# Performance work log

Measured on AMD Instinct MI355X. Metric: run time of the kernel, lower is better.

## Reference

```python
import jax, jax.numpy as jnp
import numpy as np

D_IN, D_K, D_V, BLOCK = 1024, 64, 64, 2048
B, T = 4, 2048

def setup_inputs() -> dict:
    key = jax.random.key(0)
    k0, k1, k2, k3 = jax.random.split(key, 4)
    x = jax.random.normal(k0, (B, T, D_IN), dtype=jnp.float32)
    s = 1.0 / np.sqrt(D_IN)
    Wq = jax.random.normal(k1, (D_IN, D_K), dtype=jnp.float32) * s
    Wk = jax.random.normal(k2, (D_IN, D_K), dtype=jnp.float32) * s
    Wv = jax.random.normal(k3, (D_IN, D_V), dtype=jnp.float32) * s
    return {"x": x, "Wq": Wq, "Wk": Wk, "Wv": Wv}

def reference(x, Wq, Wk, Wv):
    # Q,K,V projections (Linear without bias)
    Q = jnp.einsum('btc,ck->btk', x, Wq)
    K = jnp.einsum('btc,ck->btk', x, Wk)
    V = jnp.einsum('btc,cv->btv', x, Wv)
    Tq = x.shape[1]
    scores = jnp.einsum('bqk,btk->bqt', Q, K)  # [B,T,T]
    causal = jnp.tril(jnp.ones((Tq, Tq), dtype=bool))
    scores = jnp.where(causal, scores, -jnp.inf)
    attn = jax.nn.softmax(scores, axis=-1)
    # NOTE: original divides the AV product by sqrt(d_k) AFTER softmax
    out = jnp.einsum('bqt,btv->bqv', attn, V) / jnp.sqrt(jnp.asarray(K.shape[-1], dtype=x.dtype))
    return out
```

## Files before the change

### kernel.cpp

```cpp
#include <hip/hip_runtime.h>
#include <math.h>

typedef unsigned short u16;
typedef __attribute__((ext_vector_type(4))) float f32x4;
typedef __bf16 bf16x8 __attribute__((ext_vector_type(8)));

#define MFMA16(a,b,c) __builtin_amdgcn_mfma_f32_16x16x32_bf16((a),(b),(c),0,0,0)

typedef const __attribute__((address_space(1))) unsigned GU;
typedef __attribute__((address_space(3))) unsigned LU;
__device__ __forceinline__ void gl_lds16(const void* g, void* l) {
    __builtin_amdgcn_global_load_lds((GU*)g, (LU*)l, 16, 0, 0);
}

__device__ __forceinline__ u16 f2b(float f) {
    __bf16 h = (__bf16)f;
    return __builtin_bit_cast(u16, h);
}
__device__ __forceinline__ float b2f(u16 u) {
    unsigned v = (unsigned)u << 16;
    return __builtin_bit_cast(float, v);
}

__global__ __launch_bounds__(128) void wtrans_kernel(
    const float* __restrict__ Wq, const float* __restrict__ Wk,
    const float* __restrict__ Wv, u16* __restrict__ Wt2)
{
    const int n = blockIdx.x;
    const float* W = (n < 64) ? Wq : ((n < 128) ? Wk : Wv);
    const int nc = n & 63, cg = n >> 4, r = n & 15;
    const int t = threadIdx.x;
    const int k0 = t * 8;
    const int kstep = k0 >> 6, kh = (k0 >> 5) & 1, kg = (k0 >> 3) & 3;
    u16 hh[8], ll[8];
#pragma unroll
    for (int i = 0; i < 8; ++i) {
        const float a = W[(size_t)(k0 + i) * 64 + nc];
        hh[i] = f2b(a);
        ll[i] = f2b(a - b2f(hh[i]));
    }
    const size_t fi = (((size_t)kstep * 12 + cg) * 2 + kh) * 2;
    u16* dst = Wt2 + fi * 512 + kg * 128 + r * 8;
    uint4 vh, vl;
    vh.x = (uint)hh[0] | ((uint)hh[1] << 16); vh.y = (uint)hh[2] | ((uint)hh[3] << 16);
    vh.z = (uint)hh[4] | ((uint)hh[5] << 16); vh.w = (uint)hh[6] | ((uint)hh[7] << 16);
    vl.x = (uint)ll[0] | ((uint)ll[1] << 16); vl.y = (uint)ll[2] | ((uint)ll[3] << 16);
    vl.z = (uint)ll[4] | ((uint)ll[5] << 16); vl.w = (uint)ll[6] | ((uint)ll[7] << 16);
    *(uint4*)dst         = vh;
    *(uint4*)(dst + 512) = vl;
}

__global__ __launch_bounds__(512, 2) void proj_kernel(
    const float* __restrict__ x, const u16* __restrict__ Wt2,
    u16* __restrict__ Qhi, u16* __restrict__ Qlo,
    u16* __restrict__ Khi, u16* __restrict__ Klo, u16* __restrict__ Vt)
{
    __shared__ u16 WB[2][24576];
    __shared__ u16 vs[32][72];

    const int t = threadIdx.x, w = t >> 6, lane = t & 63;
    const int lo = lane & 15, hi = lane >> 4;
    const int mh = w & 1, nt = w >> 1;
    const int row0 = blockIdx.x * 32;

    f32x4 acc[3];
#pragma unroll
    for (int i = 0; i < 3; ++i) acc[i] = (f32x4){0.f, 0.f, 0.f, 0.f};

    const float* xrow = x + (size_t)(row0 + mh * 16 + lo) * 1024 + hi * 8;

    auto stage = [&](int buf, int step) {
        const u16* src = Wt2 + (size_t)step * 24576 + (size_t)(w * 6) * 512 + (size_t)lane * 8;
        u16* dst = &WB[buf][(w * 6) * 512];
#pragma unroll
        for (int i = 0; i < 6; ++i)
            gl_lds16(src + i * 512, dst + i * 512);
    };
    auto loadXf = [&](float4 (&xv)[2][2], int step) {
#pragma unroll
        for (int kh = 0; kh < 2; ++kh) {
            xv[kh][0] = *(const float4*)(xrow + step * 64 + kh * 32);
            xv[kh][1] = *(const float4*)(xrow + step * 64 + kh * 32 + 4);
        }
    };
    auto compute = [&](int buf, const float4 (&xv)[2][2]) {
        bf16x8 ah[2], al[2];
#pragma unroll
        for (int kh = 0; kh < 2; ++kh)
#pragma unroll
            for (int j = 0; j < 2; ++j)
#pragma unroll
                for (int c = 0; c < 4; ++c) {
                    const float f = (&xv[kh][j].x)[c];
                    const __bf16 h = (__bf16)f;
                    ah[kh][j * 4 + c] = h;
                    al[kh][j * 4 + c] = (__bf16)(f - (float)h);
                }
        const char* base = (const char*)&WB[buf][0];
#pragma unroll
        for (int i = 0; i < 3; ++i) {
            const int cg = nt * 3 + i;
#pragma unroll
            for (int kh = 0; kh < 2; ++kh) {
                const int fb = ((cg * 2 + kh) * 2) * 1024;
                const bf16x8 wh = *(const bf16x8*)(base + fb + lane * 16);
                const bf16x8 wl = *(const bf16x8*)(base + fb + 1024 + lane * 16);
                acc[i] = MFMA16(ah[kh], wh, acc[i]);
                acc[i] = MFMA16(ah[kh], wl, acc[i]);
                acc[i] = MFMA16(al[kh], wh, acc[i]);
            }
        }
    };

    float4 xA[2][2], xB[2][2];
    stage(0, 0);
    loadXf(xA, 0);
    __syncthreads();
    int buf = 0;
    for (int step = 0; step < 16; ++step) {
        if (step < 15) { stage(buf ^ 1, step + 1); loadXf(xB, step + 1); }
        compute(buf, xA);
        __syncthreads();
        if (step < 15) {
#pragma unroll
            for (int kh = 0; kh < 2; ++kh) { xA[kh][0] = xB[kh][0]; xA[kh][1] = xB[kh][1]; }
        }
        buf ^= 1;
    }

#pragma unroll
    for (int i = 0; i < 3; ++i) {
        const int cg = nt * 3 + i;
#pragma unroll
        for (int r = 0; r < 4; ++r) {
            const float v = acc[i][r];
            const int row = row0 + mh * 16 + hi * 4 + r;
            const u16 h = f2b(v);
            if (cg < 4) {
                Qhi[(size_t)row * 64 + cg * 16 + lo] = h;
                Qlo[(size_t)row * 64 + cg * 16 + lo] = f2b(v - b2f(h));
            } else if (cg < 8) {
                Khi[(size_t)row * 64 + (cg - 4) * 16 + lo] = h;
                Klo[(size_t)row * 64 + (cg - 4) * 16 + lo] = f2b(v - b2f(h));
            } else {
                vs[mh * 16 + hi * 4 + r][(cg - 8) * 16 + lo] = h;
            }
        }
    }
    __syncthreads();
    {
        const int bb = row0 >> 11, tok0 = row0 & 2047;
        const int d = t >> 3, part = t & 7;
        u16 tmp[4];
#pragma unroll
        for (int i = 0; i < 4; ++i) tmp[i] = vs[part * 4 + i][d];
        uint2 v2;
        v2.x = (uint)tmp[0] | ((uint)tmp[1] << 16);
        v2.y = (uint)tmp[2] | ((uint)tmp[3] << 16);
        *(uint2*)(Vt + (size_t)bb * 131072 + (size_t)d * 2048 + tok0 + part * 4) = v2;
    }
}

__global__ __launch_bounds__(512, 2) void attn_kernel(
    const u16* __restrict__ Qhi, const u16* __restrict__ Qlo,
    const u16* __restrict__ Khi, const u16* __restrict__ Klo,
    const u16* __restrict__ Vt, float* __restrict__ out)
{
    __shared__ u16 P[8][16 * 64];
    __shared__ float OA[8][16][64];
    __shared__ float LS[8][16];

    const int pi = blockIdx.x, b = blockIdx.y;
    const int t = threadIdx.x, w = t >> 6, l = t & 63;
    const int lo = l & 15, hi = l >> 4;

    const u16* Qh = Qhi + (size_t)b * 131072;
    const u16* Ql = Qlo + (size_t)b * 131072;
    const u16* Kh = Khi + (size_t)b * 131072;
    const u16* Kl = Klo + (size_t)b * 131072;
    const u16* V  = Vt  + (size_t)b * 131072;

    u16* Pw = P[w];

#pragma unroll 1
    for (int phase = 0; phase < 2; ++phase) {
        const int p = phase ? pi : (127 - pi);
        const int q0 = p * 16;
        const int nt = (p >> 2) + 1;

        bf16x8 aqh[2], aql[2];
#pragma unroll
        for (int s = 0; s < 2; ++s) {
            aqh[s] = *(const bf16x8*)(Qh + (size_t)(q0 + lo) * 64 + s * 32 + hi * 8);
            aql[s] = *(const bf16x8*)(Ql + (size_t)(q0 + lo) * 64 + s * 32 + hi * 8);
        }

        f32x4 acc[4];
        float ls[4];
#pragma unroll
        for (int r = 0; r < 4; ++r) { acc[r] = (f32x4){0.f,0.f,0.f,0.f}; ls[r] = 0.f; }

        bf16x8 kh[4][2], kl[4][2];
        auto loadK = [&](int j0) {
#pragma unroll
            for (int kg = 0; kg < 4; ++kg)
#pragma unroll
                for (int s = 0; s < 2; ++s) {
                    const size_t off = (size_t)(j0 + kg * 16 + lo) * 64 + s * 32 + hi * 8;
                    kh[kg][s] = *(const bf16x8*)(Kh + off);
                    kl[kg][s] = *(const bf16x8*)(Kl + off);
                }
        };

        if (w < nt) loadK(w * 64);
#pragma unroll 1
        for (int j = w; j < nt; j += 8) {
            const int j0 = j * 64;
            bf16x8 bv[4][2];
#pragma unroll
            for (int dg = 0; dg < 4; ++dg)
#pragma unroll
                for (int s = 0; s < 2; ++s)
                    bv[dg][s] = *(const bf16x8*)(V + (size_t)(dg * 16 + lo) * 2048 + j0 + s * 32 + hi * 8);

            f32x4 S[4];
            const f32x4 zf = (f32x4){0.f,0.f,0.f,0.f};
#pragma unroll
            for (int kg = 0; kg < 4; ++kg) {
                f32x4 sv = zf;
                sv = MFMA16(aqh[0], kh[kg][0], sv);
                sv = MFMA16(aqh[1], kh[kg][1], sv);
                sv = MFMA16(aqh[0], kl[kg][0], sv);
                sv = MFMA16(aqh[1], kl[kg][1], sv);
                sv = MFMA16(aql[0], kh[kg][0], sv);
                sv = MFMA16(aql[1], kh[kg][1], sv);
                S[kg] = sv;
            }

            if (j + 8 < nt) loadK((j + 8) * 64);

            const bool dm = (j == nt - 1);
#pragma unroll
            for (int r = 0; r < 4; ++r) {
                const int row = q0 + hi * 4 + r;
                float sv0 = S[0][r], sv1 = S[1][r], sv2 = S[2][r], sv3 = S[3][r];
                if (dm) {
                    sv0 = (j0 +      lo > row) ? -INFINITY : sv0;
                    sv1 = (j0 + 16 + lo > row) ? -INFINITY : sv1;
                    sv2 = (j0 + 32 + lo > row) ? -INFINITY : sv2;
                    sv3 = (j0 + 48 + lo > row) ? -INFINITY : sv3;
                }
                const u16 u0 = f2b(__expf(sv0)), u1 = f2b(__expf(sv1));
                const u16 u2 = f2b(__expf(sv2)), u3 = f2b(__expf(sv3));
                float ps = b2f(u0) + b2f(u1) + b2f(u2) + b2f(u3);
#pragma unroll
                for (int msk = 8; msk; msk >>= 1) ps += __shfl_xor(ps, msk, 64);
                ls[r] += ps;
                const int rowL = hi * 4 + r;
                const int base = rowL * 64;
                const int sw = rowL & 7;
                Pw[base + (((0 + (lo >> 3)) ^ sw) << 3) + (lo & 7)] = u0;
                Pw[base + (((2 + (lo >> 3)) ^ sw) << 3) + (lo & 7)] = u1;
                Pw[base + (((4 + (lo >> 3)) ^ sw) << 3) + (lo & 7)] = u2;
                Pw[base + (((6 + (lo >> 3)) ^ sw) << 3) + (lo & 7)] = u3;
            }
            const bf16x8 pa0 = *(const bf16x8*)&Pw[lo * 64 + (((hi    ) ^ (lo & 7)) << 3)];
            const bf16x8 pa1 = *(const bf16x8*)&Pw[lo * 64 + (((hi + 4) ^ (lo & 7)) << 3)];
#pragma unroll
            for (int dg = 0; dg < 4; ++dg) {
                acc[dg] = MFMA16(pa0, bv[dg][0], acc[dg]);
                acc[dg] = MFMA16(pa1, bv[dg][1], acc[dg]);
            }
        }

#pragma unroll
        for (int r = 0; r < 4; ++r) {
            if (lo == 0) LS[w][hi * 4 + r] = ls[r];
#pragma unroll
            for (int dg = 0; dg < 4; ++dg) OA[w][hi * 4 + r][dg * 16 + lo] = acc[dg][r];
        }
        __syncthreads();

        {
            const int row = t >> 5, c0 = (t & 31) * 2;
            float s0 = 0.f, s1 = 0.f, Lt = 0.f;
#pragma unroll
            for (int wv = 0; wv < 8; ++wv) {
                s0 += OA[wv][row][c0];
                s1 += OA[wv][row][c0 + 1];
                Lt += LS[wv][row];
            }
            const float inv = 0.125f / Lt;
            float2 o = make_float2(s0 * inv, s1 * inv);
            *(float2*)(out + ((size_t)b * 2048 + q0 + row) * 64 + c0) = o;
        }
        __syncthreads();
    }
}

extern "C" void kernel_launch(void* const* d_in, const int* in_sizes, int n_in,
                              void* d_out, int out_size, void* d_ws, size_t ws_size,
                              hipStream_t stream) {
    const float* x  = (const float*)d_in[0];
    const float* Wq = (const float*)d_in[1];
    const float* Wk = (const float*)d_in[2];
    const float* Wv = (const float*)d_in[3];
    float* outp = (float*)d_out;

    u16* Wt2 = (u16*)d_ws;
    u16* Qhi = Wt2 + 393216;
    u16* Qlo = Qhi + 524288;
    u16* Khi = Qlo + 524288;
    u16* Klo = Khi + 524288;
    u16* Vt  = Klo + 524288;

    wtrans_kernel<<<dim3(192), dim3(128), 0, stream>>>(Wq, Wk, Wv, Wt2);
    proj_kernel<<<dim3(256), dim3(512), 0, stream>>>(x, Wt2, Qhi, Qlo, Khi, Klo, Vt);
    attn_kernel<<<dim3(64, 4), dim3(512), 0, stream>>>(Qhi, Qlo, Khi, Klo, Vt, outp);
}
```

Before: 67.32 us.

## Halve projection K-step staging to cut LDS and raise occupancy

The projection kernel now stages half a K-step (32 columns) of the split hi/lo weights per iteration instead of 64. This halves the LDS double buffer to about 48KB and lets launch bounds request 4 blocks per CU instead of 2. The price is twice as many loop iterations and barriers, each with less MFMA work to hide latency behind. Register pressure may also tighten under the higher occupancy target.

```diff
diff --git a/kernel.cpp b/kernel.cpp
--- a/kernel.cpp
+++ b/kernel.cpp
@@ -2,6 +2,7 @@
 #include <math.h>
 
 typedef unsigned short u16;
+typedef unsigned int uint32;
 typedef __attribute__((ext_vector_type(4))) float f32x4;
 typedef __bf16 bf16x8 __attribute__((ext_vector_type(8)));
 
@@ -50,91 +51,82 @@
     *(uint4*)(dst + 512) = vl;
 }
 
-__global__ __launch_bounds__(512, 2) void proj_kernel(
+__global__ __launch_bounds__(512, 4) void proj_kernel(
     const float* __restrict__ x, const u16* __restrict__ Wt2,
     u16* __restrict__ Qhi, u16* __restrict__ Qlo,
     u16* __restrict__ Khi, u16* __restrict__ Klo, u16* __restrict__ Vt)
 {
-    __shared__ u16 WB[2][24576];
+    __shared__ u16 WB[2][24][512];
     __shared__ u16 vs[32][72];
 
     const int t = threadIdx.x, w = t >> 6, lane = t & 63;
     const int lo = lane & 15, hi = lane >> 4;
-    const int mh = w & 1, nt = w >> 1;
+    const int rh = w & 1, cq = w >> 1;
     const int row0 = blockIdx.x * 32;
 
     f32x4 acc[3];
 #pragma unroll
     for (int i = 0; i < 3; ++i) acc[i] = (f32x4){0.f, 0.f, 0.f, 0.f};
 
-    const float* xrow = x + (size_t)(row0 + mh * 16 + lo) * 1024 + hi * 8;
-
-    auto stage = [&](int buf, int step) {
-        const u16* src = Wt2 + (size_t)step * 24576 + (size_t)(w * 6) * 512 + (size_t)lane * 8;
-        u16* dst = &WB[buf][(w * 6) * 512];
-#pragma unroll
-        for (int i = 0; i < 6; ++i)
-            gl_lds16(src + i * 512, dst + i * 512);
+    const float* xrow = x + (size_t)(row0 + rh * 16 + lo) * 1024 + hi * 8;
+
+    auto stage = [&](int buf, int s) {
+        const int kstep = s >> 1, kh = s & 1;
+#pragma unroll
+        for (int i = 0; i < 3; ++i) {
+            const int j = w * 3 + i;
+            const int cg = j >> 1, hl = j & 1;
+            const int fi = ((kstep * 12 + cg) * 2 + kh) * 2 + hl;
+            gl_lds16(Wt2 + (size_t)fi * 512 + lane * 8, &WB[buf][j][0]);
+        }
     };
-    auto loadXf = [&](float4 (&xv)[2][2], int step) {
-#pragma unroll
-        for (int kh = 0; kh < 2; ++kh) {
-            xv[kh][0] = *(const float4*)(xrow + step * 64 + kh * 32);
-            xv[kh][1] = *(const float4*)(xrow + step * 64 + kh * 32 + 4);
-        }
+    auto loadX = [&](float4 (&xv)[2], int s) {
+        xv[0] = *(const float4*)(xrow + s * 32);
+        xv[1] = *(const float4*)(xrow + s * 32 + 4);
     };
-    auto compute = [&](int buf, const float4 (&xv)[2][2]) {
-        bf16x8 ah[2], al[2];
-#pragma unroll
-        for (int kh = 0; kh < 2; ++kh)
-#pragma unroll
-            for (int j = 0; j < 2; ++j)
-#pragma unroll
-                for (int c = 0; c < 4; ++c) {
-                    const float f = (&xv[kh][j].x)[c];
-                    const __bf16 h = (__bf16)f;
-                    ah[kh][j * 4 + c] = h;
-                    al[kh][j * 4 + c] = (__bf16)(f - (float)h);
-                }
-        const char* base = (const char*)&WB[buf][0];
+    auto compute = [&](int buf, const float4 (&xv)[2]) {
+        bf16x8 ah, al;
+#pragma unroll
+        for (int j = 0; j < 2; ++j)
+#pragma unroll
+            for (int c = 0; c < 4; ++c) {
+                const float f = (&xv[j].x)[c];
+                const __bf16 h = (__bf16)f;
+                ah[j * 4 + c] = h;
+                al[j * 4 + c] = (__bf16)(f - (float)h);
+            }
 #pragma unroll
         for (int i = 0; i < 3; ++i) {
-            const int cg = nt * 3 + i;
-#pragma unroll
-            for (int kh = 0; kh < 2; ++kh) {
-                const int fb = ((cg * 2 + kh) * 2) * 1024;
-                const bf16x8 wh = *(const bf16x8*)(base + fb + lane * 16);
-                const bf16x8 wl = *(const bf16x8*)(base + fb + 1024 + lane * 16);
-                acc[i] = MFMA16(ah[kh], wh, acc[i]);
-                acc[i] = MFMA16(ah[kh], wl, acc[i]);
-                acc[i] = MFMA16(al[kh], wh, acc[i]);
-            }
+            const int cg = cq * 3 + i;
+            const bf16x8 wh = *(const bf16x8*)((const char*)&WB[buf][cg * 2][0] + lane * 16);
+            const bf16x8 wl = *(const bf16x8*)((const char*)&WB[buf][cg * 2 + 1][0] + lane * 16);
+            acc[i] = MFMA16(ah, wh, acc[i]);
+            acc[i] = MFMA16(ah, wl, acc[i]);
+            acc[i] = MFMA16(al, wh, acc[i]);
         }
     };
 
-    float4 xA[2][2], xB[2][2];
+    float4 xA[2], xB[2];
     stage(0, 0);
-    loadXf(xA, 0);
+    loadX(xA, 0);
     __syncthreads();
     int buf = 0;
-    for (int step = 0; step < 16; ++step) {
-        if (step < 15) { stage(buf ^ 1, step + 1); loadXf(xB, step + 1); }
+#pragma unroll 1
+    for (int s = 0; s < 32; ++s) {
+        if (s < 31) { stage(buf ^ 1, s + 1); loadX(xB, s + 1); }
         compute(buf, xA);
         __syncthreads();
-        if (step < 15) {
-#pragma unroll
-            for (int kh = 0; kh < 2; ++kh) { xA[kh][0] = xB[kh][0]; xA[kh][1] = xB[kh][1]; }
-        }
+        xA[0] = xB[0]; xA[1] = xB[1];
         buf ^= 1;
     }
 
 #pragma unroll
     for (int i = 0; i < 3; ++i) {
-        const int cg = nt * 3 + i;
+        const int cg = cq * 3 + i;
 #pragma unroll
         for (int r = 0; r < 4; ++r) {
             const float v = acc[i][r];
-            const int row = row0 + mh * 16 + hi * 4 + r;
+            const int row = row0 + rh * 16 + hi * 4 + r;
             const u16 h = f2b(v);
             if (cg < 4) {
                 Qhi[(size_t)row * 64 + cg * 16 + lo] = h;
@@ -143,7 +135,7 @@
                 Khi[(size_t)row * 64 + (cg - 4) * 16 + lo] = h;
                 Klo[(size_t)row * 64 + (cg - 4) * 16 + lo] = f2b(v - b2f(h));
             } else {
-                vs[mh * 16 + hi * 4 + r][(cg - 8) * 16 + lo] = h;
+                vs[rh * 16 + hi * 4 + r][(cg - 8) * 16 + lo] = h;
             }
         }
     }
```

Measured after the change: 78.00 us. 1.16x slower.

## Triple-buffer projection K-loop with explicit vmcnt waits and batched LDS reads

Applied to the files above, without the earlier changes.

The projection kernel's weight staging moves from double to triple buffering. Global x loads and LDS weight reads are issued through inline asm, and explicit s_waitcnt vmcnt counts keep two steps of loads in flight, replacing the full __syncthreads per step with a raw s_barrier. All 12 weight fragments are read from LDS up front, before the MFMA chain runs. LDS use grows by half and the launch-bounds occupancy hint of 2 is dropped, which may lower occupancy, and the hand-counted vmcnt values are fragile.

```diff
diff --git a/kernel.cpp b/kernel.cpp
--- a/kernel.cpp
+++ b/kernel.cpp
@@ -2,7 +2,9 @@
 #include <math.h>
 
 typedef unsigned short u16;
+typedef unsigned int uint32;
 typedef __attribute__((ext_vector_type(4))) float f32x4;
+typedef __attribute__((ext_vector_type(4))) unsigned int u32x4;
 typedef __bf16 bf16x8 __attribute__((ext_vector_type(8)));
 
 #define MFMA16(a,b,c) __builtin_amdgcn_mfma_f32_16x16x32_bf16((a),(b),(c),0,0,0)
@@ -21,6 +23,17 @@
     unsigned v = (unsigned)u << 16;
     return __builtin_bit_cast(float, v);
 }
+
+__device__ __forceinline__ void agload4(f32x4& d, const float* p) {
+    asm volatile("global_load_dwordx4 %0, %1, off" : "=&v"(d) : "v"(p) : "memory");
+}
+__device__ __forceinline__ void dsr(bf16x8& d, uint32 a) {
+    u32x4 tmp;
+    asm volatile("ds_read_b128 %0, %1" : "=&v"(tmp) : "v"(a) : "memory");
+    d = __builtin_bit_cast(bf16x8, tmp);
+}
+#define WAITVM_I(n) asm volatile("s_waitcnt vmcnt(" #n ")" ::: "memory")
+#define WAITVM(n) WAITVM_I(n)
 
 __global__ __launch_bounds__(128) void wtrans_kernel(
     const float* __restrict__ Wq, const float* __restrict__ Wk,
@@ -39,7 +52,7 @@
         hh[i] = f2b(a);
         ll[i] = f2b(a - b2f(hh[i]));
     }
-    const size_t fi = (((size_t)kstep * 12 + cg) * 2 + kh) * 2;
+    const size_t fi = (size_t)kstep * 48 + (size_t)cg * 4 + (size_t)kh * 2;
     u16* dst = Wt2 + fi * 512 + kg * 128 + r * 8;
     uint4 vh, vl;
     vh.x = (uint)hh[0] | ((uint)hh[1] << 16); vh.y = (uint)hh[2] | ((uint)hh[3] << 16);
@@ -50,12 +63,12 @@
     *(uint4*)(dst + 512) = vl;
 }
 
-__global__ __launch_bounds__(512, 2) void proj_kernel(
+__global__ __launch_bounds__(512) void proj_kernel(
     const float* __restrict__ x, const u16* __restrict__ Wt2,
     u16* __restrict__ Qhi, u16* __restrict__ Qlo,
     u16* __restrict__ Khi, u16* __restrict__ Klo, u16* __restrict__ Vt)
 {
-    __shared__ u16 WB[2][24576];
+    __shared__ u16 WB[3][48][512];
     __shared__ u16 vs[32][72];
 
     const int t = threadIdx.x, w = t >> 6, lane = t & 63;
@@ -68,65 +81,74 @@
     for (int i = 0; i < 3; ++i) acc[i] = (f32x4){0.f, 0.f, 0.f, 0.f};
 
     const float* xrow = x + (size_t)(row0 + mh * 16 + lo) * 1024 + hi * 8;
-
-    auto stage = [&](int buf, int step) {
-        const u16* src = Wt2 + (size_t)step * 24576 + (size_t)(w * 6) * 512 + (size_t)lane * 8;
-        u16* dst = &WB[buf][(w * 6) * 512];
+    const uint32 ldsbase = (uint32)(size_t)(LU*)(&WB[0][0][0]);
+
+    f32x4 xr[3][4];
+
+    auto stageS = [&](int buf, int s) {
 #pragma unroll
         for (int i = 0; i < 6; ++i)
-            gl_lds16(src + i * 512, dst + i * 512);
+            gl_lds16(Wt2 + ((size_t)s * 48 + w * 6 + i) * 512 + lane * 8,
+                     &WB[buf][w * 6 + i][0]);
     };
-    auto loadXf = [&](float4 (&xv)[2][2], int step) {
+    auto issueX = [&](f32x4 (&xv)[4], int s) {
+#pragma unroll
+        for (int kh = 0; kh < 2; ++kh)
+#pragma unroll
+            for (int j = 0; j < 2; ++j)
+                agload4(xv[kh * 2 + j], xrow + s * 64 + kh * 32 + j * 4);
+    };
+    auto computeS = [&](int buf, const f32x4 (&xv)[4]) {
+        bf16x8 wf[12];
+        const uint32 bb = ldsbase + (uint32)buf * 49152u
+                        + (uint32)(nt * 12) * 1024u + (uint32)lane * 16u;
+#pragma unroll
+        for (int j = 0; j < 12; ++j)
+            dsr(wf[j], bb + (uint32)j * 1024u);
+        asm volatile("s_waitcnt lgkmcnt(0)" ::: "memory");
+        __builtin_amdgcn_sched_barrier(0);
 #pragma unroll
         for (int kh = 0; kh < 2; ++kh) {
-            xv[kh][0] = *(const float4*)(xrow + step * 64 + kh * 32);
-            xv[kh][1] = *(const float4*)(xrow + step * 64 + kh * 32 + 4);
+            bf16x8 ah, al;
+#pragma unroll
+            for (int e = 0; e < 4; ++e) {
+                { float v = xv[kh * 2][e];     __bf16 hb = (__bf16)v; ah[e] = hb;     al[e] = (__bf16)(v - (float)hb); }
+                { float v = xv[kh * 2 + 1][e]; __bf16 hb = (__bf16)v; ah[4 + e] = hb; al[4 + e] = (__bf16)(v - (float)hb); }
+            }
+#pragma unroll
+            for (int i = 0; i < 3; ++i) {
+                const bf16x8 wh = wf[i * 4 + kh * 2 + 0];
+                const bf16x8 wl = wf[i * 4 + kh * 2 + 1];
+                acc[i] = MFMA16(ah, wh, acc[i]);
+                acc[i] = MFMA16(ah, wl, acc[i]);
+                acc[i] = MFMA16(al, wh, acc[i]);
+            }
         }
     };
-    auto compute = [&](int buf, const float4 (&xv)[2][2]) {
-        bf16x8 ah[2], al[2];
-#pragma unroll
-        for (int kh = 0; kh < 2; ++kh)
-#pragma unroll
-            for (int j = 0; j < 2; ++j)
-#pragma unroll
-                for (int c = 0; c < 4; ++c) {
-                    const float f = (&xv[kh][j].x)[c];
-                    const __bf16 h = (__bf16)f;
-                    ah[kh][j * 4 + c] = h;
-                    al[kh][j * 4 + c] = (__bf16)(f - (float)h);
-                }
-        const char* base = (const char*)&WB[buf][0];
-#pragma unroll
-        for (int i = 0; i < 3; ++i) {
-            const int cg = nt * 3 + i;
-#pragma unroll
-            for (int kh = 0; kh < 2; ++kh) {
-                const int fb = ((cg * 2 + kh) * 2) * 1024;
-                const bf16x8 wh = *(const bf16x8*)(base + fb + lane * 16);
-                const bf16x8 wl = *(const bf16x8*)(base + fb + 1024 + lane * 16);
-                acc[i] = MFMA16(ah[kh], wh, acc[i]);
-                acc[i] = MFMA16(ah[kh], wl, acc[i]);
-                acc[i] = MFMA16(al[kh], wh, acc[i]);
-            }
-        }
-    };
-
-    float4 xA[2][2], xB[2][2];
-    stage(0, 0);
-    loadXf(xA, 0);
-    __syncthreads();
-    int buf = 0;
-    for (int step = 0; step < 16; ++step) {
-        if (step < 15) { stage(buf ^ 1, step + 1); loadXf(xB, step + 1); }
-        compute(buf, xA);
-        __syncthreads();
-        if (step < 15) {
-#pragma unroll
-            for (int kh = 0; kh < 2; ++kh) { xA[kh][0] = xB[kh][0]; xA[kh][1] = xB[kh][1]; }
-        }
-        buf ^= 1;
-    }
+
+    stageS(0, 0);
+    issueX(xr[0], 0);
+    stageS(1, 1);
+    issueX(xr[1], 1);
+
+#define PSTEP(S_, N1_)                                                  \
+    do {                                                                \
+        WAITVM(N1_);                                                    \
+        __builtin_amdgcn_sched_barrier(0);                              \
+        __builtin_amdgcn_s_barrier();                                   \
+        __builtin_amdgcn_sched_barrier(0);                              \
+        if ((S_) + 2 <= 15) {                                           \
+            stageS(((S_) + 2) % 3, (S_) + 2);                           \
+            issueX(xr[((S_) + 2) % 3], (S_) + 2);                       \
+        }                                                               \
+        computeS((S_) % 3, xr[(S_) % 3]);                               \
+    } while (0)
+
+    PSTEP(0, 10);  PSTEP(1, 10);  PSTEP(2, 10);  PSTEP(3, 10);
+    PSTEP(4, 10);  PSTEP(5, 10);  PSTEP(6, 10);  PSTEP(7, 10);
+    PSTEP(8, 10);  PSTEP(9, 10);  PSTEP(10, 10); PSTEP(11, 10);
+    PSTEP(12, 10); PSTEP(13, 10); PSTEP(14, 10); PSTEP(15, 0);
+#undef PSTEP
 
 #pragma unroll
     for (int i = 0; i < 3; ++i) {
```

Result: faster. 62.09 us (-7.8%).
